# Performance work log

Measured on AMD Instinct MI355X. Metric: run time of the kernel, lower is better.

Reference implementation:

```python
import jax, jax.numpy as jnp
import numpy as np

T, B, D, H = 2048, 64, 256, 512  # seq_len, batch, input_size, hidden_size


def setup_inputs() -> dict:
    key = jax.random.key(0)
    k0, k1, k2 = jax.random.split(key, 3)
    x = jax.random.normal(k0, (T, B, D), dtype=jnp.float32)
    # fused gate weights for i, f, g, o gates (standard LSTM block graph)
    Wx = jax.random.normal(k1, (D, 4 * H), dtype=jnp.float32) / np.sqrt(D)
    Wh = jax.random.normal(k2, (H, 4 * H), dtype=jnp.float32) / np.sqrt(H)
    b = jnp.zeros((4 * H,), dtype=jnp.float32)
    return {"x": x, "Wx": Wx, "Wh": Wh, "b": b}


def reference(x, Wx, Wh, b):
    # Faithful translation of the 'ptb' forward branch: time-major scan over
    # torch.unbind(input, dim=0), per-step gate linears + sigmoid/tanh blocks,
    # h/c state threading, outputs stacked along time.
    Bt = x.shape[1]
    Hh = Wh.shape[0]
    h0 = jnp.zeros((Bt, Hh), dtype=x.dtype)
    c0 = jnp.zeros((Bt, Hh), dtype=x.dtype)

    def step(carry, x_t):
        h, c = carry
        gates = x_t @ Wx + h @ Wh + b  # [B, 4H]
        i, f, g, o = jnp.split(gates, 4, axis=-1)
        i = jax.nn.sigmoid(i)
        f = jax.nn.sigmoid(f)
        g = jnp.tanh(g)
        o = jax.nn.sigmoid(o)
        c_next = f * c + i * g
        h_next = o * jnp.tanh(c_next)
        return (h_next, c_next), h_next

    (h_T, c_T), ys = jax.lax.scan(step, (h0, c0), x)
    return ys, (h_T, c_T)
```

## Files before the change

kernel.cpp:

```cpp
#include <hip/hip_runtime.h>
#include <stdint.h>

#define T_STEPS 2048
#define NBATCH  64
#define DIN     256
#define HID     512
#define NCOL    2048
#define LDK     776
#define NGRP    8
#define BPG     32
#define MROW    8
#define SENT    0xFFFFFFFFu

#define HBUF_DWORDS ((size_t)4 * NBATCH * (HID / 2))

typedef __attribute__((ext_vector_type(8))) short bf16x8;
typedef __attribute__((ext_vector_type(4))) float f32x4;

static __device__ __forceinline__ ushort f2bf(float f) {
    union { float f; uint32_t u; } v; v.f = f;
    uint32_t r = v.u + 0x7FFFu + ((v.u >> 16) & 1u);
    return (ushort)(r >> 16);
}
static __device__ __forceinline__ float sigm(float x) { return 1.f / (1.f + __expf(-x)); }
static __device__ __forceinline__ float tanh_fast(float x) {
    float a = fabsf(x);
    float e = __expf(-2.f * a);
    float t = (1.f - e) / (1.f + e);
    return x < 0.f ? -t : t;
}
static __device__ __forceinline__ unsigned long long ldq(const unsigned long long* p) {
    return __hip_atomic_load(p, __ATOMIC_RELAXED, __HIP_MEMORY_SCOPE_AGENT);
}
static __device__ __forceinline__ bool chk64(unsigned long long v) {
    return ((uint32_t)v != SENT) && ((uint32_t)(v >> 32) != SENT);
}

__global__ void sent_fill_kernel(uint32_t* w, size_t n) {
    size_t i = (size_t)blockIdx.x * blockDim.x + threadIdx.x;
    if (i < n) w[i] = SENT;
}

__global__ __launch_bounds__(256, 1) void lstm_persist(
    const float* __restrict__ x,
    const float* __restrict__ Wx,
    const float* __restrict__ Wh,
    const float* __restrict__ bias,
    float* __restrict__ out,
    uint32_t* __restrict__ hbuf)
{
    __shared__ __align__(16) ushort zlds[16][LDK];
    __shared__ __align__(16) float gex[8][17][4];

    const int tid  = threadIdx.x;
    const int gid  = blockIdx.x & 7;
    const int p    = blockIdx.x >> 3;
    const int j0   = p * 16;
    const int gb   = gid * MROW;
    const int wave = tid >> 6;
    const int lane = tid & 63;

    for (int i = tid; i < 8 * LDK; i += 256) zlds[8 + i / LDK][i % LDK] = 0;

    bf16x8 wreg[24];
    {
        const int col   = wave * HID + j0 + (lane & 15);
        const int kbase = (lane >> 4) * 8;
        #pragma unroll
        for (int ch = 0; ch < 24; ++ch) {
            bf16x8 w;
            #pragma unroll
            for (int e = 0; e < 8; ++e) {
                int k = ch * 32 + kbase + e;
                float wv = (k < DIN) ? Wx[(size_t)k * NCOL + col]
                                     : Wh[(size_t)(k - DIN) * NCOL + col];
                w[e] = (short)f2bf(wv);
            }
            wreg[ch] = w;
        }
    }
    const float biasv = bias[wave * HID + j0 + (lane & 15)];
    float c0 = 0.f, c1 = 0.f;
    __syncthreads();

    const int xr   = tid >> 5;
    const int xc   = (tid & 31) * 8;
    const int arow = lane & 15;
    const int koff = (lane >> 4) * 8;
    const ushort* za = &zlds[arow][0];
    const int hr = wave * 2;

    float4 xa, xb;
    {
        const float* xp = x + ((size_t)0 * NBATCH + gb + xr) * DIN + xc;
        xa = *(const float4*)xp;
        xb = *(const float4*)(xp + 4);
    }

    for (int t = 0; t < T_STEPS; ++t) {
        {
            uint4 pk;
            pk.x = (uint32_t)f2bf(xa.x) | ((uint32_t)f2bf(xa.y) << 16);
            pk.y = (uint32_t)f2bf(xa.z) | ((uint32_t)f2bf(xa.w) << 16);
            pk.z = (uint32_t)f2bf(xb.x) | ((uint32_t)f2bf(xb.y) << 16);
            pk.w = (uint32_t)f2bf(xb.z) | ((uint32_t)f2bf(xb.w) << 16);
            *(uint4*)&zlds[xr][xc] = pk;
        }
        __syncthreads();

        const unsigned long long* hq =
            (const unsigned long long*)(hbuf + ((size_t)(t & 3) * NBATCH + gb + hr) * (HID / 2))
            + 2 * lane;
        const unsigned long long* hq2 = hq + (HID / 4);
        unsigned long long pa0 = 0, pa1 = 0, pb0 = 0, pb1 = 0;
        if (t > 0) {
            pa0 = ldq(hq);  pa1 = ldq(hq + 1);
            pb0 = ldq(hq2); pb1 = ldq(hq2 + 1);
        }

        {
            int tn = (t + 1 < T_STEPS) ? t + 1 : t;
            const float* xp = x + ((size_t)tn * NBATCH + gb + xr) * DIN + xc;
            xa = *(const float4*)xp;
            xb = *(const float4*)(xp + 4);
        }

        f32x4 a0 = {0.f, 0.f, 0.f, 0.f};
        #pragma unroll
        for (int ch = 0; ch < 8; ++ch) {
            bf16x8 af = *(const bf16x8*)(za + ch * 32 + koff);
            a0 = __builtin_amdgcn_mfma_f32_16x16x32_bf16(af, wreg[ch], a0, 0, 0, 0);
        }

        if (t > 0) {
            int guard = 0;
            while (true) {
                bool ok = chk64(pa0) && chk64(pa1) && chk64(pb0) && chk64(pb1);
                if (__all((int)ok)) break;
                if (++guard > (1 << 17)) break;
                pa0 = ldq(hq);  pa1 = ldq(hq + 1);
                pb0 = ldq(hq2); pb1 = ldq(hq2 + 1);
            }
            uint4 q0, q1;
            q0.x = (uint32_t)pa0; q0.y = (uint32_t)(pa0 >> 32);
            q0.z = (uint32_t)pa1; q0.w = (uint32_t)(pa1 >> 32);
            q1.x = (uint32_t)pb0; q1.y = (uint32_t)(pb0 >> 32);
            q1.z = (uint32_t)pb1; q1.w = (uint32_t)(pb1 >> 32);
            *(uint4*)&zlds[hr][DIN + 8 * lane]     = q0;
            *(uint4*)&zlds[hr + 1][DIN + 8 * lane] = q1;
        } else {
            uint4 z4 = {0u, 0u, 0u, 0u};
            *(uint4*)&zlds[hr][DIN + 8 * lane]     = z4;
            *(uint4*)&zlds[hr + 1][DIN + 8 * lane] = z4;
        }

        if (tid < 64) {
            const int b = tid >> 3, jp = tid & 7;
            __hip_atomic_store(hbuf + ((size_t)((t + 2) & 3) * NBATCH + gb + b) * (HID / 2)
                               + (j0 >> 1) + jp, SENT,
                               __ATOMIC_RELAXED, __HIP_MEMORY_SCOPE_AGENT);
        }
        __syncthreads();

        f32x4 a1 = {0.f, 0.f, 0.f, 0.f};
        f32x4 a2 = {0.f, 0.f, 0.f, 0.f};
        f32x4 a3 = {0.f, 0.f, 0.f, 0.f};
        f32x4 a4 = {0.f, 0.f, 0.f, 0.f};
        #pragma unroll
        for (int ch = 8; ch < 12; ++ch) {
            bf16x8 af = *(const bf16x8*)(za + ch * 32 + koff);
            a1 = __builtin_amdgcn_mfma_f32_16x16x32_bf16(af, wreg[ch], a1, 0, 0, 0);
        }
        #pragma unroll
        for (int ch = 12; ch < 16; ++ch) {
            bf16x8 af = *(const bf16x8*)(za + ch * 32 + koff);
            a2 = __builtin_amdgcn_mfma_f32_16x16x32_bf16(af, wreg[ch], a2, 0, 0, 0);
        }
        #pragma unroll
        for (int ch = 16; ch < 20; ++ch) {
            bf16x8 af = *(const bf16x8*)(za + ch * 32 + koff);
            a3 = __builtin_amdgcn_mfma_f32_16x16x32_bf16(af, wreg[ch], a3, 0, 0, 0);
        }
        #pragma unroll
        for (int ch = 20; ch < 24; ++ch) {
            bf16x8 af = *(const bf16x8*)(za + ch * 32 + koff);
            a4 = __builtin_amdgcn_mfma_f32_16x16x32_bf16(af, wreg[ch], a4, 0, 0, 0);
        }
        f32x4 acc = ((a0 + a1) + (a2 + a3)) + a4;

        if (lane < 32) {
            int r0 = (lane >> 4) * 4, col = lane & 15;
            #pragma unroll
            for (int r = 0; r < 4; ++r)
                gex[r0 + r][col][wave] = acc[r] + biasv;
        }
        __syncthreads();

        if (tid < 64) {
            const int b = tid >> 3, jp = tid & 7, j = jp * 2;
            f32x4 ga = *(const f32x4*)&gex[b][j][0];
            f32x4 gc = *(const f32x4*)&gex[b][j + 1][0];
            float i0 = sigm(ga[0]), f0 = sigm(ga[1]), g0 = tanh_fast(ga[2]), o0 = sigm(ga[3]);
            float i1 = sigm(gc[0]), f1 = sigm(gc[1]), g1 = tanh_fast(gc[2]), o1 = sigm(gc[3]);
            c0 = f0 * c0 + i0 * g0;
            c1 = f1 * c1 + i1 * g1;
            float h0v = o0 * tanh_fast(c0);
            float h1v = o1 * tanh_fast(c1);

            uint32_t pkh = (uint32_t)f2bf(h0v) | ((uint32_t)f2bf(h1v) << 16);
            __hip_atomic_store(hbuf + ((size_t)((t + 1) & 3) * NBATCH + gb + b) * (HID / 2)
                               + (j0 >> 1) + jp, pkh,
                               __ATOMIC_RELAXED, __HIP_MEMORY_SCOPE_AGENT);

            float2 hv = {h0v, h1v};
            *(float2*)(out + ((size_t)t * NBATCH + gb + b) * HID + j0 + j) = hv;
            if (t == T_STEPS - 1) {
                float* hTp = out + (size_t)T_STEPS * NBATCH * HID
                             + (size_t)(gb + b) * HID + j0 + j;
                float2 cv = {c0, c1};
                *(float2*)hTp = hv;
                *(float2*)(hTp + (size_t)NBATCH * HID) = cv;
            }
        }
    }
}

extern "C" void kernel_launch(void* const* d_in, const int* in_sizes, int n_in,
                              void* d_out, int out_size, void* d_ws, size_t ws_size,
                              hipStream_t stream) {
    const float* x    = (const float*)d_in[0];
    const float* Wx   = (const float*)d_in[1];
    const float* Wh   = (const float*)d_in[2];
    const float* bias = (const float*)d_in[3];
    float* out = (float*)d_out;

    uint32_t* hbuf = (uint32_t*)d_ws;

    {
        size_t n = HBUF_DWORDS;
        int blocks = (int)((n + 255) / 256);
        sent_fill_kernel<<<dim3(blocks), dim3(256), 0, stream>>>(hbuf, n);
    }
    lstm_persist<<<dim3(NGRP * BPG), dim3(256), 0, stream>>>(x, Wx, Wh, bias, out, hbuf);
}
```

Measured before the change: 4.012 ms.

## Remap gate columns so each wave owns all four gates and drop block barrier

Weight columns are re-permuted so each wave's 16 MFMA output columns hold the i,f,g,o gates for 4 hidden units. The per-wave gate results can then go through a wave-private LDS area and into the cell update with no block-wide __syncthreads. The aim is to remove one barrier per time step from the serial recurrence and spread the elementwise work across all waves. In exchange it adds shuffles to pack h pairs and more, narrower stores per wave.

Measured after the change: 4.107 ms. 2.3% more time.

```diff
diff --git a/kernel.cpp b/kernel.cpp
--- a/kernel.cpp
+++ b/kernel.cpp
@@ -50,7 +50,7 @@
     uint32_t* __restrict__ hbuf)
 {
     __shared__ __align__(16) ushort zlds[16][LDK];
-    __shared__ __align__(16) float gex[8][17][4];
+    __shared__ __align__(16) float gexw[4][8][17];
 
     const int tid  = threadIdx.x;
     const int gid  = blockIdx.x & 7;
@@ -64,7 +64,9 @@
 
     bf16x8 wreg[24];
     {
-        const int col   = wave * HID + j0 + (lane & 15);
+        const int q     = (lane & 15) >> 2;
+        const int r     = lane & 3;
+        const int col   = q * HID + j0 + 4 * wave + r;
         const int kbase = (lane >> 4) * 8;
         #pragma unroll
         for (int ch = 0; ch < 24; ++ch) {
@@ -79,8 +81,10 @@
             wreg[ch] = w;
         }
     }
-    const float biasv = bias[wave * HID + j0 + (lane & 15)];
-    float c0 = 0.f, c1 = 0.f;
+    const float biasv = bias[((lane & 15) >> 2) * HID + j0 + 4 * wave + (lane & 3)];
+    const int ub = lane >> 2;
+    const int jr = lane & 3;
+    float creg = 0.f;
     __syncthreads();
 
     const int xr   = tid >> 5;
@@ -112,10 +116,9 @@
             (const unsigned long long*)(hbuf + ((size_t)(t & 3) * NBATCH + gb + hr) * (HID / 2))
             + 2 * lane;
         const unsigned long long* hq2 = hq + (HID / 4);
-        unsigned long long pa0 = 0, pa1 = 0, pb0 = 0, pb1 = 0;
+        unsigned long long pa0 = 0, pa1 = 0, pa2 = 0, pa3 = 0;
         if (t > 0) {
-            pa0 = ldq(hq);  pa1 = ldq(hq + 1);
-            pb0 = ldq(hq2); pb1 = ldq(hq2 + 1);
+            pa0 = ldq(hq); pa1 = ldq(hq + 1); pa2 = ldq(hq2); pa3 = ldq(hq2 + 1);
         }
 
         {
@@ -135,17 +138,16 @@
         if (t > 0) {
             int guard = 0;
             while (true) {
-                bool ok = chk64(pa0) && chk64(pa1) && chk64(pb0) && chk64(pb1);
+                bool ok = chk64(pa0) && chk64(pa1) && chk64(pa2) && chk64(pa3);
                 if (__all((int)ok)) break;
                 if (++guard > (1 << 17)) break;
-                pa0 = ldq(hq);  pa1 = ldq(hq + 1);
-                pb0 = ldq(hq2); pb1 = ldq(hq2 + 1);
+                pa0 = ldq(hq); pa1 = ldq(hq + 1); pa2 = ldq(hq2); pa3 = ldq(hq2 + 1);
             }
             uint4 q0, q1;
             q0.x = (uint32_t)pa0; q0.y = (uint32_t)(pa0 >> 32);
             q0.z = (uint32_t)pa1; q0.w = (uint32_t)(pa1 >> 32);
-            q1.x = (uint32_t)pb0; q1.y = (uint32_t)(pb0 >> 32);
-            q1.z = (uint32_t)pb1; q1.w = (uint32_t)(pb1 >> 32);
+            q1.x = (uint32_t)pa2; q1.y = (uint32_t)(pa2 >> 32);
+            q1.z = (uint32_t)pa3; q1.w = (uint32_t)(pa3 >> 32);
             *(uint4*)&zlds[hr][DIN + 8 * lane]     = q0;
             *(uint4*)&zlds[hr + 1][DIN + 8 * lane] = q1;
         } else {
@@ -154,10 +156,9 @@
             *(uint4*)&zlds[hr + 1][DIN + 8 * lane] = z4;
         }
 
-        if (tid < 64) {
-            const int b = tid >> 3, jp = tid & 7;
-            __hip_atomic_store(hbuf + ((size_t)((t + 2) & 3) * NBATCH + gb + b) * (HID / 2)
-                               + (j0 >> 1) + jp, SENT,
+        if (lane < 16) {
+            __hip_atomic_store(hbuf + ((size_t)((t + 2) & 3) * NBATCH + gb + (lane >> 1)) * (HID / 2)
+                               + (j0 >> 1) + 2 * wave + (lane & 1), SENT,
                                __ATOMIC_RELAXED, __HIP_MEMORY_SCOPE_AGENT);
         }
         __syncthreads();
@@ -192,34 +193,36 @@
             int r0 = (lane >> 4) * 4, col = lane & 15;
             #pragma unroll
             for (int r = 0; r < 4; ++r)
-                gex[r0 + r][col][wave] = acc[r] + biasv;
-        }
-        __syncthreads();
-
-        if (tid < 64) {
-            const int b = tid >> 3, jp = tid & 7, j = jp * 2;
-            f32x4 ga = *(const f32x4*)&gex[b][j][0];
-            f32x4 gc = *(const f32x4*)&gex[b][j + 1][0];
-            float i0 = sigm(ga[0]), f0 = sigm(ga[1]), g0 = tanh_fast(ga[2]), o0 = sigm(ga[3]);
-            float i1 = sigm(gc[0]), f1 = sigm(gc[1]), g1 = tanh_fast(gc[2]), o1 = sigm(gc[3]);
-            c0 = f0 * c0 + i0 * g0;
-            c1 = f1 * c1 + i1 * g1;
-            float h0v = o0 * tanh_fast(c0);
-            float h1v = o1 * tanh_fast(c1);
-
-            uint32_t pkh = (uint32_t)f2bf(h0v) | ((uint32_t)f2bf(h1v) << 16);
-            __hip_atomic_store(hbuf + ((size_t)((t + 1) & 3) * NBATCH + gb + b) * (HID / 2)
-                               + (j0 >> 1) + jp, pkh,
-                               __ATOMIC_RELAXED, __HIP_MEMORY_SCOPE_AGENT);
-
-            float2 hv = {h0v, h1v};
-            *(float2*)(out + ((size_t)t * NBATCH + gb + b) * HID + j0 + j) = hv;
+                gexw[wave][r0 + r][col] = acc[r] + biasv;
+        }
+
+        if (lane < 32) {
+            float iv = sigm(gexw[wave][ub][0 * 4 + jr]);
+            float fv = sigm(gexw[wave][ub][1 * 4 + jr]);
+            float gv = tanh_fast(gexw[wave][ub][2 * 4 + jr]);
+            float ov = sigm(gexw[wave][ub][3 * 4 + jr]);
+            creg = fv * creg + iv * gv;
+            float hv = ov * tanh_fast(creg);
+
+            float nh = __shfl_xor(hv, 1);
+            if ((lane & 1) == 0) {
+                uint32_t pkh = (uint32_t)f2bf(hv) | ((uint32_t)f2bf(nh) << 16);
+                __hip_atomic_store(hbuf + ((size_t)((t + 1) & 3) * NBATCH + gb + ub) * (HID / 2)
+                                   + (j0 >> 1) + 2 * wave + (jr >> 1), pkh,
+                                   __ATOMIC_RELAXED, __HIP_MEMORY_SCOPE_AGENT);
+                float2 hv2 = {hv, nh};
+                *(float2*)(out + ((size_t)t * NBATCH + gb + ub) * HID + j0 + 4 * wave + jr) = hv2;
+            }
             if (t == T_STEPS - 1) {
-                float* hTp = out + (size_t)T_STEPS * NBATCH * HID
-                             + (size_t)(gb + b) * HID + j0 + j;
-                float2 cv = {c0, c1};
-                *(float2*)hTp = hv;
-                *(float2*)(hTp + (size_t)NBATCH * HID) = cv;
+                float nc = __shfl_xor(creg, 1);
+                if ((lane & 1) == 0) {
+                    float* hTp = out + (size_t)T_STEPS * NBATCH * HID
+                                 + (size_t)(gb + ub) * HID + j0 + 4 * wave + jr;
+                    float2 hv2 = {hv, nh};
+                    float2 cv2 = {creg, nc};
+                    *(float2*)hTp = hv2;
+                    *(float2*)(hTp + (size_t)NBATCH * HID) = cv2;
+                }
             }
         }
     }
```
